# Optimization experiments

Hardware: AMD Instinct MI355X
Metric: run time of the kernel (lower is better)

Reference implementation:

```python
import jax, jax.numpy as jnp
import numpy as np

B, L, S, D, H = 32, 256, 64, 128, 4
DH = D // H
EPS = 1e-5


def _uniform(k, shape, scale):
    return jax.random.uniform(k, shape, jnp.float32, -scale, scale)


def setup_inputs() -> dict:
    key = jax.random.key(0)
    ks = jax.random.split(key, 12)
    sc = 1.0 / np.sqrt(D)
    return {
        "h_wq": jax.random.normal(ks[0], (B, L, D), jnp.float32),
        "h_all": jax.random.normal(ks[1], (B, L, S, D), jnp.float32),
        "station_id": jax.random.randint(ks[2], (B,), 0, S),
        "adj": jax.random.randint(ks[3], (S, S), 0, 2).astype(jnp.float32),
        "in_proj_w": _uniform(ks[4], (3 * D, D), sc),
        "in_proj_b": _uniform(ks[5], (3 * D,), sc),
        "out_w": _uniform(ks[6], (D, D), sc),
        "out_b": _uniform(ks[7], (D,), sc),
        "gate_w": _uniform(ks[8], (D, 2 * D), 1.0 / np.sqrt(2 * D)),
        "gate_b": _uniform(ks[9], (D,), 1.0 / np.sqrt(2 * D)),
        "ln_g": jnp.ones((D,), jnp.float32),
        "ln_b": jnp.zeros((D,), jnp.float32),
        "alpha": jnp.asarray(0.1, jnp.float32),
    }


def _allowed_mask(adj, station_id):
    # allowed[b, s] == True  <=> station s may attend as key for sample b
    sid = station_id.astype(jnp.int32)
    allowed = adj[sid] > 0.0                                  # [B, S]
    self_oh = jax.nn.one_hot(sid, adj.shape[0], dtype=bool)   # [B, S]
    allowed = allowed & ~self_oh                              # exclude self
    # fallback-to-all for rows with no neighbor (still excluding self)
    no_nb = ~jnp.any(allowed, axis=1, keepdims=True)
    allowed = jnp.where(no_nb, ~self_oh, allowed)
    # final safety: if STILL empty (S==1 edge case), allow self
    no_nb2 = ~jnp.any(allowed, axis=1, keepdims=True)
    allowed = allowed | (no_nb2 & self_oh)
    return allowed


def _forward(h_wq, h_all, station_id, adj, in_proj_w, in_proj_b,
             out_w, out_b, gate_w, gate_b, ln_g, ln_b, alpha):
    b, l, d = h_wq.shape
    s = h_all.shape[2]
    qw, kw, vw = jnp.split(in_proj_w, 3, axis=0)
    qb, kb, vb = jnp.split(in_proj_b, 3, axis=0)

    q = (h_wq @ qw.T + qb).reshape(b, l, H, DH)        # [B,L,H,DH]
    k = (h_all @ kw.T + kb).reshape(b, l, s, H, DH)    # [B,L,S,H,DH]
    v = (h_all @ vw.T + vb).reshape(b, l, s, H, DH)

    scores = jnp.einsum('blhd,blshd->blhs', q, k) / np.sqrt(DH)  # [B,L,H,S]
    allowed = _allowed_mask(adj, station_id)                     # [B,S]
    scores = jnp.where(allowed[:, None, None, :], scores, -jnp.inf)
    w = jax.nn.softmax(scores, axis=-1)

    ctx = jnp.einsum('blhs,blshd->blhd', w, v).reshape(b, l, d)
    ctx = ctx @ out_w.T + out_b                                  # out_proj

    g = jax.nn.sigmoid(jnp.concatenate([h_wq, ctx], axis=-1) @ gate_w.T + gate_b)
    y = h_wq + alpha * (g * ctx)                                 # dropout = eval mode

    mu = jnp.mean(y, axis=-1, keepdims=True)
    var = jnp.mean(jnp.square(y - mu), axis=-1, keepdims=True)
    return (y - mu) * jax.lax.rsqrt(var + EPS) * ln_g + ln_b


def reference(h_wq, h_all, station_id, adj, in_proj_w, in_proj_b,
              out_w, out_b, gate_w, gate_b, ln_g, ln_b, alpha):
    return _forward(h_wq, h_all, station_id, adj, in_proj_w, in_proj_b,
                    out_w, out_b, gate_w, gate_b, ln_g, ln_b, alpha)
```

## Files before the change

### kernel.cpp

```cpp
#include <hip/hip_runtime.h>
#include <math.h>

#define B_   32
#define L_   256
#define S_   64
#define D_   128
#define H_   4
#define DH_  32
#define NTOK (B_*L_)

#define QK_OFF   0
#define QK_BYTES ((size_t)NTOK*512*4)
#define CB_OFF   (QK_OFF + QK_BYTES)
#define CB_BYTES ((size_t)NTOK*4*4)
#define CTX_OFF  (CB_OFF + CB_BYTES)

__global__ __launch_bounds__(256) void qk_kernel(
        const float* __restrict__ h_wq,
        const float* __restrict__ in_proj_w, const float* __restrict__ in_proj_b,
        float* __restrict__ qk_out, float* __restrict__ cb_out) {
    __shared__ float x_lds[32*128];
    __shared__ float q_lds[32*128];
    const int t0 = blockIdx.x * 32;
    const int tid = threadIdx.x;

    {
        const float4* src = (const float4*)(h_wq + (size_t)t0*128);
        float4* dst = (float4*)x_lds;
        for (int e = tid; e < 32*32; e += 256) dst[e] = src[e];
    }
    __syncthreads();

    const int d = tid & 127, half = tid >> 7;
    const float* xb = x_lds + half*16*128;
    {
        float acc[16];
        const float qb = in_proj_b[d];
        #pragma unroll
        for (int t = 0; t < 16; ++t) acc[t] = qb;
        const float4* wrow = (const float4*)(in_proj_w + (size_t)d*128);
        for (int j4 = 0; j4 < 32; ++j4) {
            float4 w = wrow[j4];
            #pragma unroll
            for (int t = 0; t < 16; ++t) {
                float4 x = *(const float4*)(xb + t*128 + j4*4);
                acc[t] += w.x*x.x + w.y*x.y + w.z*x.z + w.w*x.w;
            }
        }
        #pragma unroll
        for (int t = 0; t < 16; ++t) q_lds[(half*16+t)*128 + d] = acc[t];
    }
    __syncthreads();

    const float scale = 0.17677669529663687f;
    const float* qbse = q_lds + half*16*128;
    #pragma unroll
    for (int h = 0; h < 4; ++h) {
        float acc[16];
        #pragma unroll
        for (int t = 0; t < 16; ++t) acc[t] = 0.f;
        for (int j = 0; j < 32; ++j) {
            float w = in_proj_w[(size_t)(128 + h*32 + j)*128 + d];
            #pragma unroll
            for (int t = 0; t < 16; ++t) acc[t] += w * qbse[t*128 + h*32 + j];
        }
        #pragma unroll
        for (int t = 0; t < 16; ++t)
            qk_out[(size_t)(t0 + half*16 + t)*512 + h*128 + d] = acc[t] * scale;
    }
    if (tid < 128) {
        int t = tid >> 2, h = tid & 3;
        float s = 0.f;
        for (int j = 0; j < 32; ++j)
            s += q_lds[t*128 + h*32 + j] * in_proj_b[128 + h*32 + j];
        cb_out[(t0 + t)*4 + h] = s * scale;
    }
}

__global__ __launch_bounds__(128) void attn_kernel(
        const float* __restrict__ h_all,
        const float* __restrict__ in_proj_w, const float* __restrict__ in_proj_b,
        const float* __restrict__ qk_buf, const float* __restrict__ cb_buf,
        const int* __restrict__ station_id, const float* __restrict__ adj,
        float* __restrict__ ctx_out) {
    __shared__ float qk_lds[4*132];
    __shared__ float sc[4*64];
    __shared__ float u_lds[4*128];
    __shared__ int   lst[64];
    __shared__ int   cnt_s;
    __shared__ float cb[4];

    const int t = blockIdx.x;
    const int b = t >> 8;
    const int tid = threadIdx.x;

    #pragma unroll
    for (int h = 0; h < 4; ++h)
        qk_lds[h*132 + tid] = qk_buf[(size_t)t*512 + h*128 + tid];
    if (tid < 4) cb[tid] = cb_buf[t*4 + tid];

    if (tid < 64) {
        int sid = station_id[b];
        int s = tid;
        bool av = (adj[sid*S_ + s] > 0.0f) && (s != sid);
        unsigned long long m = __ballot(av);
        if (m == 0ull) { av = (s != sid); m = __ballot(av); }
        if (m == 0ull) { av = (s == sid); m = __ballot(av); }
        int idx = __popcll(m & ((1ull << s) - 1ull));
        if (av) lst[idx] = s;
        if (s == 0) cnt_s = __popcll(m);
    }
    __syncthreads();
    const int cnt = cnt_s;
    const float* rowbase = h_all + (size_t)t * (S_*D_);

    for (int p = tid; p < 4*cnt; p += 128) {
        int h = p & 3, i = p >> 2;
        float acc = cb[h];
        const float4* qr = (const float4*)(qk_lds + h*132);
        const float4* rr = (const float4*)(rowbase + lst[i]*D_);
        #pragma unroll 8
        for (int j = 0; j < 32; ++j) {
            float4 a = qr[j], x = rr[j];
            acc += a.x*x.x + a.y*x.y + a.z*x.z + a.w*x.w;
        }
        sc[h*64 + i] = acc;
    }
    __syncthreads();

    {
        int h = tid >> 5, j = tid & 31;
        float v0 = (j < cnt)      ? sc[h*64 + j]      : -INFINITY;
        float v1 = (j + 32 < cnt) ? sc[h*64 + j + 32] : -INFINITY;
        float m = fmaxf(v0, v1);
        for (int o = 16; o >= 1; o >>= 1) m = fmaxf(m, __shfl_xor(m, o, 32));
        float e0 = (j < cnt)      ? __expf(v0 - m) : 0.f;
        float e1 = (j + 32 < cnt) ? __expf(v1 - m) : 0.f;
        float ssum = e0 + e1;
        for (int o = 16; o >= 1; o >>= 1) ssum += __shfl_xor(ssum, o, 32);
        float inv = 1.0f / ssum;
        sc[h*64 + j]      = e0 * inv;
        sc[h*64 + j + 32] = e1 * inv;
    }
    __syncthreads();

    {
        float u0=0.f, u1=0.f, u2=0.f, u3=0.f;
        for (int i = 0; i < cnt; ++i) {
            float xv = rowbase[lst[i]*D_ + tid];
            u0 += sc[i]       * xv;
            u1 += sc[64 + i]  * xv;
            u2 += sc[128 + i] * xv;
            u3 += sc[192 + i] * xv;
        }
        u_lds[tid] = u0; u_lds[128+tid] = u1; u_lds[256+tid] = u2; u_lds[384+tid] = u3;
    }
    __syncthreads();

    {
        int h = tid >> 5;
        const float4* vwrow = (const float4*)(in_proj_w + (size_t)(256 + tid)*128);
        const float4* ur = (const float4*)(u_lds + h*128);
        float acc = in_proj_b[256 + tid];
        #pragma unroll 8
        for (int j = 0; j < 32; ++j) {
            float4 w = vwrow[j], u = ur[j];
            acc += w.x*u.x + w.y*u.y + w.z*u.z + w.w*u.w;
        }
        ctx_out[(size_t)t*128 + tid] = acc;
    }
}

__global__ __launch_bounds__(256) void epi_kernel(
        const float* __restrict__ h_wq, const float* __restrict__ ctx_buf,
        const float* __restrict__ out_w, const float* __restrict__ out_b,
        const float* __restrict__ gate_w, const float* __restrict__ gate_b,
        const float* __restrict__ ln_g, const float* __restrict__ ln_b,
        const float* __restrict__ alpha, float* __restrict__ out) {
    __shared__ float c_tile[32*128];
    __shared__ float x_tile[32*128];
    __shared__ float o_tile[32*128];
    __shared__ float mu_s[32], rs_s[32];
    const int t0 = blockIdx.x * 32;
    const int tid = threadIdx.x;

    {
        const float4* cs = (const float4*)(ctx_buf + (size_t)t0*128);
        const float4* xs = (const float4*)(h_wq + (size_t)t0*128);
        float4* cd = (float4*)c_tile; float4* xd = (float4*)x_tile;
        for (int e = tid; e < 32*32; e += 256) { cd[e] = cs[e]; xd[e] = xs[e]; }
    }
    __syncthreads();

    const int d = tid & 127, half = tid >> 7;
    float o_acc[16];
    {
        const float ob = out_b[d];
        #pragma unroll
        for (int t = 0; t < 16; ++t) o_acc[t] = ob;
        const float4* wrow = (const float4*)(out_w + (size_t)d*128);
        const float* cbp = c_tile + half*16*128;
        for (int j4 = 0; j4 < 32; ++j4) {
            float4 w = wrow[j4];
            #pragma unroll
            for (int t = 0; t < 16; ++t) {
                float4 c = *(const float4*)(cbp + t*128 + j4*4);
                o_acc[t] += w.x*c.x + w.y*c.y + w.z*c.z + w.w*c.w;
            }
        }
        #pragma unroll
        for (int t = 0; t < 16; ++t) o_tile[(half*16+t)*128 + d] = o_acc[t];
    }
    __syncthreads();

    {
        float g_acc[16];
        const float gb = gate_b[d];
        #pragma unroll
        for (int t = 0; t < 16; ++t) g_acc[t] = gb;
        const float4* wrow = (const float4*)(gate_w + (size_t)d*256);
        const float* xb = x_tile + half*16*128;
        const float* obp = o_tile + half*16*128;
        for (int j4 = 0; j4 < 32; ++j4) {
            float4 w0 = wrow[j4];
            float4 w1 = wrow[32 + j4];
            #pragma unroll
            for (int t = 0; t < 16; ++t) {
                float4 x = *(const float4*)(xb  + t*128 + j4*4);
                float4 o = *(const float4*)(obp + t*128 + j4*4);
                g_acc[t] += w0.x*x.x + w0.y*x.y + w0.z*x.z + w0.w*x.w
                          + w1.x*o.x + w1.y*o.y + w1.z*o.z + w1.w*o.w;
            }
        }
        const float al = alpha[0];
        #pragma unroll
        for (int t = 0; t < 16; ++t) {
            float g = 1.0f / (1.0f + __expf(-g_acc[t]));
            float y = xb[t*128 + d] + al * g * o_acc[t];
            c_tile[(half*16+t)*128 + d] = y;
        }
    }
    __syncthreads();

    {
        int tt = tid >> 3, k = tid & 7;
        const float* yr = c_tile + tt*128;
        float s = 0.f;
        for (int dd = k; dd < 128; dd += 8) s += yr[dd];
        for (int o = 4; o >= 1; o >>= 1) s += __shfl_xor(s, o, 8);
        float mu = s * (1.0f/128.0f);
        float vs = 0.f;
        for (int dd = k; dd < 128; dd += 8) { float df = yr[dd] - mu; vs += df*df; }
        for (int o = 4; o >= 1; o >>= 1) vs += __shfl_xor(vs, o, 8);
        if (k == 0) { mu_s[tt] = mu; rs_s[tt] = rsqrtf(vs*(1.0f/128.0f) + 1e-5f); }
    }
    __syncthreads();

    for (int e = tid; e < 32*128; e += 256) {
        int tt = e >> 7, dd = e & 127;
        float y = c_tile[e];
        out[(size_t)t0*128 + e] = (y - mu_s[tt]) * rs_s[tt] * ln_g[dd] + ln_b[dd];
    }
}

extern "C" void kernel_launch(void* const* d_in, const int* in_sizes, int n_in,
                              void* d_out, int out_size, void* d_ws, size_t ws_size,
                              hipStream_t stream) {
    const float* h_wq       = (const float*)d_in[0];
    const float* h_all      = (const float*)d_in[1];
    const int*   station_id = (const int*)  d_in[2];
    const float* adj        = (const float*)d_in[3];
    const float* in_proj_w  = (const float*)d_in[4];
    const float* in_proj_b  = (const float*)d_in[5];
    const float* out_w      = (const float*)d_in[6];
    const float* out_b      = (const float*)d_in[7];
    const float* gate_w     = (const float*)d_in[8];
    const float* gate_b     = (const float*)d_in[9];
    const float* ln_g       = (const float*)d_in[10];
    const float* ln_b       = (const float*)d_in[11];
    const float* alpha      = (const float*)d_in[12];

    char* ws = (char*)d_ws;
    float* qk   = (float*)(ws + QK_OFF);
    float* cb   = (float*)(ws + CB_OFF);
    float* ctx  = (float*)(ws + CTX_OFF);
    float* out  = (float*)d_out;

    qk_kernel  <<<NTOK/32, 256, 0, stream>>>(h_wq, in_proj_w, in_proj_b, qk, cb);
    attn_kernel<<<NTOK, 128, 0, stream>>>(h_all, in_proj_w, in_proj_b, qk, cb,
                                          station_id, adj, ctx);
    epi_kernel <<<NTOK/32, 256, 0, stream>>>(h_wq, ctx, out_w, out_b, gate_w,
                                             gate_b, ln_g, ln_b, alpha, out);
}
```

Before: 479.1 us.

## Process four tokens per attention block with one wavefront per token

The attention kernel now handles four tokens per 256-thread block, with each 64-lane wavefront owning one token's scores, softmax and weighted sum. This removes most block-wide barriers. The final V projection is shared across the four tokens, so each in_proj_w row is loaded once and reused for four outputs. Block count drops fourfold. Each wavefront now does the per-token work that 128 threads did before, so per-token latency rises while block-level overhead and weight traffic fall.

After: 448.0 us. 6.5% less time.

```diff
diff --git a/kernel.cpp b/kernel.cpp
--- a/kernel.cpp
+++ b/kernel.cpp
@@ -77,27 +77,25 @@
     }
 }
 
-__global__ __launch_bounds__(128) void attn_kernel(
+__global__ __launch_bounds__(256) void attn_kernel(
         const float* __restrict__ h_all,
         const float* __restrict__ in_proj_w, const float* __restrict__ in_proj_b,
         const float* __restrict__ qk_buf, const float* __restrict__ cb_buf,
         const int* __restrict__ station_id, const float* __restrict__ adj,
         float* __restrict__ ctx_out) {
-    __shared__ float qk_lds[4*132];
-    __shared__ float sc[4*64];
-    __shared__ float u_lds[4*128];
+    __shared__ float qk_lds[4][4*132];
+    __shared__ float sc[4][4*64];
+    __shared__ float u_lds[4][4*132];
     __shared__ int   lst[64];
     __shared__ int   cnt_s;
-    __shared__ float cb[4];
-
-    const int t = blockIdx.x;
-    const int b = t >> 8;
+    __shared__ float cb[4][4];
+
+    const int t0  = blockIdx.x * 4;
+    const int b   = t0 >> 8;
     const int tid = threadIdx.x;
-
-    #pragma unroll
-    for (int h = 0; h < 4; ++h)
-        qk_lds[h*132 + tid] = qk_buf[(size_t)t*512 + h*128 + tid];
-    if (tid < 4) cb[tid] = cb_buf[t*4 + tid];
+    const int wv  = tid >> 6;
+    const int lane = tid & 63;
+    const int t = t0 + wv;
 
     if (tid < 64) {
         int sid = station_id[b];
@@ -110,64 +108,89 @@
         if (av) lst[idx] = s;
         if (s == 0) cnt_s = __popcll(m);
     }
-    __syncthreads();
+
+    {
+        const float4* src = (const float4*)(qk_buf + (size_t)t*512);
+        for (int e = lane; e < 128; e += 64) {
+            int h = e >> 5, d4 = e & 31;
+            *(float4*)&qk_lds[wv][h*132 + d4*4] = src[e];
+        }
+    }
+    if (lane < 4) cb[wv][lane] = cb_buf[t*4 + lane];
+    __syncthreads();
+
     const int cnt = cnt_s;
     const float* rowbase = h_all + (size_t)t * (S_*D_);
 
-    for (int p = tid; p < 4*cnt; p += 128) {
+    for (int p = lane; p < 4*cnt; p += 64) {
         int h = p & 3, i = p >> 2;
-        float acc = cb[h];
-        const float4* qr = (const float4*)(qk_lds + h*132);
+        float acc = cb[wv][h];
+        const float4* qr = (const float4*)(&qk_lds[wv][h*132]);
         const float4* rr = (const float4*)(rowbase + lst[i]*D_);
         #pragma unroll 8
         for (int j = 0; j < 32; ++j) {
             float4 a = qr[j], x = rr[j];
             acc += a.x*x.x + a.y*x.y + a.z*x.z + a.w*x.w;
         }
-        sc[h*64 + i] = acc;
-    }
-    __syncthreads();
-
-    {
-        int h = tid >> 5, j = tid & 31;
-        float v0 = (j < cnt)      ? sc[h*64 + j]      : -INFINITY;
-        float v1 = (j + 32 < cnt) ? sc[h*64 + j + 32] : -INFINITY;
-        float m = fmaxf(v0, v1);
-        for (int o = 16; o >= 1; o >>= 1) m = fmaxf(m, __shfl_xor(m, o, 32));
-        float e0 = (j < cnt)      ? __expf(v0 - m) : 0.f;
-        float e1 = (j + 32 < cnt) ? __expf(v1 - m) : 0.f;
-        float ssum = e0 + e1;
-        for (int o = 16; o >= 1; o >>= 1) ssum += __shfl_xor(ssum, o, 32);
-        float inv = 1.0f / ssum;
-        sc[h*64 + j]      = e0 * inv;
-        sc[h*64 + j + 32] = e1 * inv;
-    }
-    __syncthreads();
-
-    {
-        float u0=0.f, u1=0.f, u2=0.f, u3=0.f;
+        sc[wv][h*64 + i] = acc;
+    }
+
+    {
+        int j = lane & 31;
+        for (int h = (lane >> 5); h < 4; h += 2) {
+            float v0 = (j < cnt)      ? sc[wv][h*64 + j]      : -INFINITY;
+            float v1 = (j + 32 < cnt) ? sc[wv][h*64 + j + 32] : -INFINITY;
+            float m = fmaxf(v0, v1);
+            for (int o = 16; o >= 1; o >>= 1) m = fmaxf(m, __shfl_xor(m, o, 32));
+            float e0 = (j < cnt)      ? __expf(v0 - m) : 0.f;
+            float e1 = (j + 32 < cnt) ? __expf(v1 - m) : 0.f;
+            float ssum = e0 + e1;
+            for (int o = 16; o >= 1; o >>= 1) ssum += __shfl_xor(ssum, o, 32);
+            float inv = 1.0f / ssum;
+            sc[wv][h*64 + j]      = e0 * inv;
+            sc[wv][h*64 + j + 32] = e1 * inv;
+        }
+    }
+
+    {
+        float2 u0 = {0.f,0.f}, u1 = {0.f,0.f}, u2 = {0.f,0.f}, u3 = {0.f,0.f};
+        #pragma unroll 4
         for (int i = 0; i < cnt; ++i) {
-            float xv = rowbase[lst[i]*D_ + tid];
-            u0 += sc[i]       * xv;
-            u1 += sc[64 + i]  * xv;
-            u2 += sc[128 + i] * xv;
-            u3 += sc[192 + i] * xv;
-        }
-        u_lds[tid] = u0; u_lds[128+tid] = u1; u_lds[256+tid] = u2; u_lds[384+tid] = u3;
-    }
-    __syncthreads();
-
-    {
-        int h = tid >> 5;
-        const float4* vwrow = (const float4*)(in_proj_w + (size_t)(256 + tid)*128);
-        const float4* ur = (const float4*)(u_lds + h*128);
-        float acc = in_proj_b[256 + tid];
+            float2 x = *(const float2*)(rowbase + lst[i]*D_ + 2*lane);
+            float w0 = sc[wv][i], w1 = sc[wv][64+i], w2 = sc[wv][128+i], w3 = sc[wv][192+i];
+            u0.x += w0*x.x; u0.y += w0*x.y;
+            u1.x += w1*x.x; u1.y += w1*x.y;
+            u2.x += w2*x.x; u2.y += w2*x.y;
+            u3.x += w3*x.x; u3.y += w3*x.y;
+        }
+        *(float2*)&u_lds[wv][0*132 + 2*lane] = u0;
+        *(float2*)&u_lds[wv][1*132 + 2*lane] = u1;
+        *(float2*)&u_lds[wv][2*132 + 2*lane] = u2;
+        *(float2*)&u_lds[wv][3*132 + 2*lane] = u3;
+    }
+    __syncthreads();
+
+    if (tid < 128) {
+        const int d = tid, h = d >> 5;
+        const float4* vwrow = (const float4*)(in_proj_w + (size_t)(256 + d)*128);
+        const float vb = in_proj_b[256 + d];
+        float a0 = vb, a1 = vb, a2 = vb, a3 = vb;
         #pragma unroll 8
-        for (int j = 0; j < 32; ++j) {
-            float4 w = vwrow[j], u = ur[j];
-            acc += w.x*u.x + w.y*u.y + w.z*u.z + w.w*u.w;
-        }
-        ctx_out[(size_t)t*128 + tid] = acc;
+        for (int j4 = 0; j4 < 32; ++j4) {
+            float4 w = vwrow[j4];
+            float4 u0 = *(const float4*)(&u_lds[0][h*132 + j4*4]);
+            float4 u1 = *(const float4*)(&u_lds[1][h*132 + j4*4]);
+            float4 u2 = *(const float4*)(&u_lds[2][h*132 + j4*4]);
+            float4 u3 = *(const float4*)(&u_lds[3][h*132 + j4*4]);
+            a0 += w.x*u0.x + w.y*u0.y + w.z*u0.z + w.w*u0.w;
+            a1 += w.x*u1.x + w.y*u1.y + w.z*u1.z + w.w*u1.w;
+            a2 += w.x*u2.x + w.y*u2.y + w.z*u2.z + w.w*u2.w;
+            a3 += w.x*u3.x + w.y*u3.y + w.z*u3.z + w.w*u3.w;
+        }
+        ctx_out[(size_t)(t0+0)*128 + d] = a0;
+        ctx_out[(size_t)(t0+1)*128 + d] = a1;
+        ctx_out[(size_t)(t0+2)*128 + d] = a2;
+        ctx_out[(size_t)(t0+3)*128 + d] = a3;
     }
 }
 
@@ -287,8 +310,8 @@
     float* out  = (float*)d_out;
 
     qk_kernel  <<<NTOK/32, 256, 0, stream>>>(h_wq, in_proj_w, in_proj_b, qk, cb);
-    attn_kernel<<<NTOK, 128, 0, stream>>>(h_all, in_proj_w, in_proj_b, qk, cb,
-                                          station_id, adj, ctx);
+    attn_kernel<<<NTOK/4, 256, 0, stream>>>(h_all, in_proj_w, in_proj_b, qk, cb,
+                                            station_id, adj, ctx);
     epi_kernel <<<NTOK/32, 256, 0, stream>>>(h_wq, ctx, out_w, out_b, gate_w,
                                              gate_b, ln_g, ln_b, alpha, out);
 }
```
